# Performance work log

Hardware: AMD Instinct MI355X
Metric: run time of the kernel (lower is better)

Reference implementation:

```python
import jax, jax.numpy as jnp
import numpy as np

B, S, D = 2, 2048, 4096
NH, NKV = 32, 8
HD = D // NH          # 128
NREP = NH // NKV      # 4
SCALE = HD ** -0.5


def setup_inputs() -> dict:
    key = jax.random.key(0)
    kx, kq, kk, kv, ko = jax.random.split(key, 5)
    s = 0.02
    return {
        "x": jax.random.normal(kx, (B, S, D), dtype=jnp.float32),
        "wq": jax.random.normal(kq, (D, NH * HD), dtype=jnp.float32) * s,
        "wk": jax.random.normal(kk, (D, NKV * HD), dtype=jnp.float32) * s,
        "wv": jax.random.normal(kv, (D, NKV * HD), dtype=jnp.float32) * s,
        "wo": jax.random.normal(ko, (NH * HD, D), dtype=jnp.float32) * s,
    }


def reference(x, wq, wk, wv, wo):
    b, s, _ = x.shape
    q = (x @ wq).reshape(b, s, NH, HD)    # b s h d
    k = (x @ wk).reshape(b, s, NKV, HD)   # b s kv d
    v = (x @ wv).reshape(b, s, NKV, HD)
    # GQA: repeat kv heads to match query heads
    k = jnp.repeat(k, NREP, axis=2)       # b s h d
    v = jnp.repeat(v, NREP, axis=2)
    scores = jnp.einsum("bihd,bjhd->bhij", q, k) * SCALE  # b h i j
    causal = jnp.tril(jnp.ones((s, s), dtype=bool))
    scores = jnp.where(causal, scores, jnp.finfo(scores.dtype).min)
    attn = jax.nn.softmax(scores, axis=-1)
    out = jnp.einsum("bhij,bjhd->bihd", attn, v)          # b s h d
    out = out.reshape(b, s, NH * HD)
    return out @ wo
```

## Files before the change

### kernel.cpp

```cpp
#include <hip/hip_runtime.h>
#include <cstdint>
#include <cstddef>

typedef __bf16 bf16x8 __attribute__((ext_vector_type(8)));
typedef float  f32x4  __attribute__((ext_vector_type(4)));
typedef unsigned short u16;

#define SCALE_F 0.08838834764831845f
#define QSCALE_F (0.08838834764831845f * 1.4426950408889634f)

__device__ __forceinline__ u16 f2bf(float f) {
  unsigned int u = __builtin_bit_cast(unsigned int, f);
  u += 0x7fffu + ((u >> 16) & 1u);
  return (u16)(u >> 16);
}

__device__ __forceinline__ unsigned cvt_pk_bf16(float lo, float hi) {
  unsigned r;
  asm("v_cvt_pk_bf16_f32 %0, %1, %2" : "=v"(r) : "v"(lo), "v"(hi));
  return r;
}

__device__ __forceinline__ void load_lds16(const void* g, void* l) {
  __builtin_amdgcn_global_load_lds((const __attribute__((address_space(1))) void*)g,
                                   (__attribute__((address_space(3))) void*)l,
                                   16, 0, 0);
}

__global__ __launch_bounds__(256) void prep_all(const float* __restrict__ x,
                                                const float* __restrict__ wq,
                                                const float* __restrict__ wk,
                                                const float* __restrict__ wv,
                                                const float* __restrict__ wo,
                                                u16* __restrict__ xb,
                                                u16* __restrict__ wqkvT,
                                                u16* __restrict__ woT) {
  __shared__ float tile[32][33];
  const int tid = threadIdx.x;
  int blk = blockIdx.x;
  if (blk < 2048) {
    int idx = blk * 256 + tid;
    const int n4 = 4096 * 4096 / 4;
    for (; idx < n4; idx += 2048 * 256) {
      float4 v = ((const float4*)x)[idx];
      uint2 pk;
      pk.x = (unsigned)f2bf(v.x) | ((unsigned)f2bf(v.y) << 16);
      pk.y = (unsigned)f2bf(v.z) | ((unsigned)f2bf(v.w) << 16);
      ((uint2*)xb)[idx] = pk;
    }
    return;
  }
  blk -= 2048;
  const float* in; u16* out; long C; int nbx; float scale;
  if (blk < 16384)      { in = wq; out = wqkvT;                          C = 4096; nbx = 128; scale = QSCALE_F; }
  else if (blk < 20480) { blk -= 16384; in = wk; out = wqkvT + (size_t)4096 * 4096; C = 1024; nbx = 32; scale = 1.f; }
  else if (blk < 24576) { blk -= 20480; in = wv; out = wqkvT + (size_t)5120 * 4096; C = 1024; nbx = 32; scale = 1.f; }
  else                  { blk -= 24576; in = wo; out = woT;              C = 4096; nbx = 128; scale = 1.f; }
  const long R = 4096;
  const int tx = tid & 31, ty = tid >> 5;
  const long c0 = (long)(blk % nbx) * 32, r0 = (long)(blk / nbx) * 32;
#pragma unroll
  for (int i = 0; i < 4; i++)
    tile[ty + i * 8][tx] = in[(r0 + ty + i * 8) * C + c0 + tx];
  __syncthreads();
#pragma unroll
  for (int i = 0; i < 4; i++)
    out[(c0 + ty + i * 8) * R + r0 + tx] = f2bf(tile[tx][ty + i * 8] * scale);
}

__global__ __launch_bounds__(256) void transpose_u16(const u16* __restrict__ in,
                                                     u16* __restrict__ out,
                                                     int R, int C, int ldi, int ldo) {
  __shared__ u16 tile[32][33];
  const int tx = threadIdx.x, ty = threadIdx.y;
  const long c0 = (long)blockIdx.x * 32, r0 = (long)blockIdx.y * 32;
#pragma unroll
  for (int i = 0; i < 4; i++)
    tile[ty + i * 8][tx] = in[(r0 + ty + i * 8) * (long)ldi + c0 + tx];
  __syncthreads();
#pragma unroll
  for (int i = 0; i < 4; i++)
    out[(c0 + ty + i * 8) * (long)ldo + r0 + tx] = tile[tx][ty + i * 8];
}

#define STGA(db, ks, KC) { int kc_ = (KC) < K ? (KC) : 0; \
    load_lds16(gA0 + kc_, &SA[db][ks][s0 * 8]); \
    load_lds16(gA1 + kc_, &SA[db][ks][s1 * 8]); }
#define STGB(db, ks, KC) { int kc_ = (KC) < K ? (KC) : 0; \
    load_lds16(gB0 + kc_, &SB[db][ks][s0 * 8]); \
    load_lds16(gB1 + kc_, &SB[db][ks][s1 * 8]); }

#define PH(MBc, AU, BU, DBn, KSn, MBn, AN, RDB, BN, STG, DOVM) { \
    STG; \
    if (DOVM) asm volatile("s_waitcnt vmcnt(8)"); \
    __builtin_amdgcn_s_barrier(); \
    _Pragma("unroll") for (int mm = 0; mm < 4; mm++) \
      AN[mm] = *(const bf16x8*)(&SA[DBn][KSn][aoff + (MBn + mm) * 512]); \
    if (RDB) { \
      _Pragma("unroll") for (int n = 0; n < 4; n++) \
        BN[n] = *(const bf16x8*)(&SB[DBn][KSn][boff + n * 512]); \
    } \
    __builtin_amdgcn_s_setprio(1); \
    _Pragma("unroll") for (int mm = 0; mm < 4; mm++) \
      _Pragma("unroll") for (int n = 0; n < 4; n++) \
        acc[MBc + mm][n] = __builtin_amdgcn_mfma_f32_16x16x32_bf16(AU[mm], BU[n], acc[MBc + mm][n], 0, 0, 0); \
    __builtin_amdgcn_s_setprio(0); \
  }

template <int BF16_OUT>
__global__ __launch_bounds__(512, 2) void gemm256(const u16* __restrict__ A,
                                                  const u16* __restrict__ Bt,
                                                  void* __restrict__ Cv,
                                                  int M, int N, int K, int NBX) {
  __shared__ u16 SA[2][2][8192];
  __shared__ u16 SB[2][2][8192];
  const int tid = threadIdx.x;
  const int lane = tid & 63;
  const int g = lane >> 4, r16 = lane & 15;
  const int wid = tid >> 6;
  const int wm = wid >> 2, wn = wid & 3;

  const int cpx = gridDim.x >> 3;
  const int lin = (blockIdx.x & 7) * cpx + (blockIdx.x >> 3);
  const long bm = (long)(lin / NBX) * 256;
  const long bn = (long)(lin % NBX) * 256;

  const int s0 = tid, s1 = 512 + tid;
  const int rp0 = s0 >> 3, ci0 = (s0 & 7) ^ (rp0 & 7);
  const int rp1 = s1 >> 3, ci1 = (s1 & 7) ^ (rp1 & 7);
  const long gr0 = rp0 * 2 + (ci0 >> 2), gc0 = (ci0 & 3) * 8;
  const long gr1 = rp1 * 2 + (ci1 >> 2), gc1 = (ci1 & 3) * 8;
  const u16* gA0 = A + (bm + gr0) * K + gc0;
  const u16* gA1 = A + (bm + gr1) * K + gc1;
  const u16* gB0 = Bt + (bn + gr0) * K + gc0;
  const u16* gB1 = Bt + (bn + gr1) * K + gc1;

  const int rA = wm * 128 + r16;
  const int aoff = (rA >> 1) * 64 + ((((rA & 1) << 2) + g) ^ ((rA >> 1) & 7)) * 8;
  const int rB = wn * 64 + r16;
  const int boff = (rB >> 1) * 64 + ((((rB & 1) << 2) + g) ^ ((rB >> 1) & 7)) * 8;

  f32x4 acc[8][4];
#pragma unroll
  for (int m = 0; m < 8; m++)
#pragma unroll
    for (int n = 0; n < 4; n++)
#pragma unroll
      for (int j = 0; j < 4; j++) acc[m][n][j] = 0.f;

  bf16x8 afrX[4], afrY[4], bfrX[4], bfrY[4];

  STGA(0, 0, 0); STGB(0, 0, 0);
  STGA(0, 1, 32); STGB(0, 1, 32);
  STGA(1, 0, 64); STGB(1, 0, 64);
  __builtin_amdgcn_sched_barrier(0);
  asm volatile("s_waitcnt vmcnt(0)" ::: "memory");
  __builtin_amdgcn_s_barrier();

#pragma unroll
  for (int mm = 0; mm < 4; mm++)
    afrX[mm] = *(const bf16x8*)(&SA[0][0][aoff + mm * 512]);
#pragma unroll
  for (int n = 0; n < 4; n++)
    bfrX[n] = *(const bf16x8*)(&SB[0][0][boff + n * 512]);

  for (int it = 0; it < K / 128; it++) {
    const int t0 = it * 128;
    PH(0, afrX, bfrX, 0, 0, 4, afrY, 0, bfrY, STGA(1, 1, t0 + 96), 0);
    PH(4, afrY, bfrX, 0, 1, 0, afrX, 1, bfrY, STGB(1, 1, t0 + 96), 1);
    PH(0, afrX, bfrY, 0, 1, 4, afrY, 0, bfrX, STGA(0, 0, t0 + 128), 0);
    PH(4, afrY, bfrY, 1, 0, 0, afrX, 1, bfrX, STGB(0, 0, t0 + 128), 1);
    PH(0, afrX, bfrX, 1, 0, 4, afrY, 0, bfrY, STGA(0, 1, t0 + 160), 0);
    PH(4, afrY, bfrX, 1, 1, 0, afrX, 1, bfrY, STGB(0, 1, t0 + 160), 1);
    PH(0, afrX, bfrY, 1, 1, 4, afrY, 0, bfrX, STGA(1, 0, t0 + 192), 0);
    PH(4, afrY, bfrY, 0, 0, 0, afrX, 1, bfrX, STGB(1, 0, t0 + 192), 1);
  }

  const long crow = bm + wm * 128 + g * 4;
  const long ccol = bn + wn * 64 + r16;
  if (BF16_OUT) {
    u16* C = (u16*)Cv;
#pragma unroll
    for (int m = 0; m < 8; m++)
#pragma unroll
      for (int n = 0; n < 4; n++)
#pragma unroll
        for (int j = 0; j < 4; j++)
          C[(crow + m * 16 + j) * (long)N + ccol + n * 16] = f2bf(acc[m][n][j]);
  } else {
    float* C = (float*)Cv;
#pragma unroll
    for (int m = 0; m < 8; m++)
#pragma unroll
      for (int n = 0; n < 4; n++)
#pragma unroll
        for (int j = 0; j < 4; j++)
          C[(crow + m * 16 + j) * (long)N + ccol + n * 16] = acc[m][n][j];
  }
}

__global__ __launch_bounds__(512, 4) void attn_fwd(const u16* __restrict__ QK,
                                                   const u16* __restrict__ VT,
                                                   u16* __restrict__ Og) {
  __shared__ u16 Ks[2][64 * 128];
  __shared__ u16 Vs[2][128 * 64];
  __shared__ u16 Ps[8][16 * 64];
  const int tid = threadIdx.x;
  const int lane = tid & 63;
  const int w = tid >> 6;
  const int g = lane >> 4, r16 = lane & 15;
  const int qtA = blockIdx.x;
  const int qtB = 15 - qtA;
  const int h = blockIdx.y, b = blockIdx.z;
  const int kvh = h >> 2;

  const u16* kcol   = QK + (long)b * 2048 * 6144 + 4096 + kvh * 128;
  const u16* vb_ptr = VT + (long)kvh * 128 * 4096 + (long)b * 2048;
  u16* pw = Ps[w];

  const int nktA = 2 * (qtA + 1);
  const int ntot = 34;

  int qbase = qtA * 128;
  int qlo = qbase + w * 16;
  int qrow = qlo + r16;

  bf16x8 qf[4];
  auto load_q = [&]() {
    const u16* qp = QK + ((long)(b * 2048 + qrow)) * 6144 + h * 128 + g * 8;
#pragma unroll
    for (int kc = 0; kc < 4; kc++) qf[kc] = *(const bf16x8*)(qp + kc * 32);
  };
  load_q();

  f32x4 oacc[8];
  float mrun, lrun;
  auto reinit = [&]() {
#pragma unroll
    for (int dt = 0; dt < 8; dt++)
#pragma unroll
      for (int j = 0; j < 4; j++) oacc[dt][j] = 0.f;
    mrun = -__builtin_inff();
    lrun = 0.f;
  };
  reinit();

  auto finalize = [&]() {
    float li[4];
#pragma unroll
    for (int j = 0; j < 4; j++)
      li[j] = 1.f / __shfl(lrun, (lane & 48) + g * 4 + j);
    u16* op = Og + ((long)(b * 2048 + qbase + w * 16 + g * 4)) * 4096 + h * 128 + r16;
#pragma unroll
    for (int dt = 0; dt < 8; dt++)
#pragma unroll
      for (int j = 0; j < 4; j++)
        op[(long)j * 4096 + dt * 16] = f2bf(oacc[dt][j] * li[j]);
  };

  auto stage = [&](int bf, int kb) {
#pragma unroll
    for (int i = 0; i < 2; i++) {
      int slot = i * 512 + tid;
      int r = slot >> 4, cs = slot & 15;
      int ck = (cs & 8) | ((cs ^ r) & 7);
      load_lds16(kcol + (long)(kb + r) * 6144 + ck * 8, &Ks[bf][slot * 8]);
      int d = slot >> 3, c8 = slot & 7;
      int cv = (c8 ^ d) & 7;
      load_lds16(vb_ptr + (long)d * 4096 + kb + cv * 8, &Vs[bf][slot * 8]);
    }
  };

  stage(0, 0);
  __syncthreads();
  int cur = 0;

  for (int i = 0; i < ntot; i++) {
    if (i == nktA) {
      finalize();
      qbase = qtB * 128;
      qlo = qbase + w * 16;
      qrow = qlo + r16;
      load_q();
      reinit();
    }
    const int kt = (i < nktA) ? i : i - nktA;
    const int kb = kt * 64;
    if (i + 1 < ntot) {
      const int ktn = (i + 1 < nktA) ? i + 1 : i + 1 - nktA;
      stage(cur ^ 1, ktn * 64);
    }

    if (kb <= qlo + 15) {
      const bool masked = (kb + 63 > qlo);

      f32x4 st[4];
#pragma unroll
      for (int t = 0; t < 4; t++)
#pragma unroll
        for (int j = 0; j < 4; j++) st[t][j] = 0.f;
#pragma unroll
      for (int t = 0; t < 4; t++) {
        const int r = t * 16 + r16;
#pragma unroll
        for (int kc = 0; kc < 4; kc++) {
          int c = kc * 4 + g;
          int cz = (c & 8) | ((c ^ r) & 7);
          bf16x8 kf = *(const bf16x8*)(&Ks[cur][r * 128 + cz * 8]);
          st[t] = __builtin_amdgcn_mfma_f32_16x16x32_bf16(kf, qf[kc], st[t], 0, 0, 0);
        }
      }

      float p[4][4];
      float tmax = -__builtin_inff();
#pragma unroll
      for (int t = 0; t < 4; t++)
#pragma unroll
        for (int j = 0; j < 4; j++) {
          float s = st[t][j];
          if (masked) {
            int kv = kb + t * 16 + g * 4 + j;
            s = (kv > qrow) ? -__builtin_inff() : s;
          }
          p[t][j] = s;
          tmax = fmaxf(tmax, s);
        }
      tmax = fmaxf(tmax, __shfl_xor(tmax, 16));
      tmax = fmaxf(tmax, __shfl_xor(tmax, 32));

      if (!__all(tmax <= mrun + 8.f)) {
        const float mnew = fmaxf(mrun, tmax);
        const float esc = exp2f(mrun - mnew);
        float es[4];
#pragma unroll
        for (int j = 0; j < 4; j++) es[j] = __shfl(esc, (lane & 48) + g * 4 + j);
#pragma unroll
        for (int dt = 0; dt < 8; dt++)
#pragma unroll
          for (int j = 0; j < 4; j++) oacc[dt][j] *= es[j];
        lrun *= esc;
        mrun = mnew;
      }
      float psum = 0.f;
#pragma unroll
      for (int t = 0; t < 4; t++)
#pragma unroll
        for (int j = 0; j < 4; j++) {
          float e = exp2f(p[t][j] - mrun);
          p[t][j] = e;
          psum += e;
        }
      psum += __shfl_xor(psum, 16);
      psum += __shfl_xor(psum, 32);
      lrun += psum;

#pragma unroll
      for (int t = 0; t < 4; t++)
#pragma unroll
        for (int pp = 0; pp < 2; pp++) {
          int kvl = t * 16 + g * 4 + pp * 2;
          unsigned val = cvt_pk_bf16(p[t][pp * 2], p[t][pp * 2 + 1]);
          int off = r16 * 128 + ((kvl * 2) ^ ((r16 & 7) << 4));
          *(unsigned int*)((char*)pw + off) = val;
        }

#pragma unroll
      for (int kc2 = 0; kc2 < 2; kc2++) {
        int c = kc2 * 4 + g;
        int cp = c ^ (r16 & 7);
        bf16x8 pa = *(const bf16x8*)(pw + r16 * 64 + cp * 8);
#pragma unroll
        for (int dt = 0; dt < 8; dt++) {
          int d = dt * 16 + r16;
          int cz = c ^ (d & 7);
          bf16x8 vf = *(const bf16x8*)(&Vs[cur][d * 64 + cz * 8]);
          oacc[dt] = __builtin_amdgcn_mfma_f32_16x16x32_bf16(pa, vf, oacc[dt], 0, 0, 0);
        }
      }
    }

    __syncthreads();
    cur ^= 1;
  }

  finalize();
}

extern "C" void kernel_launch(void* const* d_in, const int* in_sizes, int n_in,
                              void* d_out, int out_size, void* d_ws, size_t ws_size,
                              hipStream_t stream) {
  (void)in_sizes; (void)n_in; (void)out_size; (void)ws_size;
  const float* x  = (const float*)d_in[0];
  const float* wq = (const float*)d_in[1];
  const float* wk = (const float*)d_in[2];
  const float* wv = (const float*)d_in[3];
  const float* wo = (const float*)d_in[4];
  float* out = (float*)d_out;

  u16* xb     = (u16*)d_ws;
  u16* wqkvT  = xb    + (size_t)4096 * 4096;
  u16* woT    = wqkvT + (size_t)6144 * 4096;
  u16* qkv    = woT   + (size_t)4096 * 4096;
  u16* vT     = qkv   + (size_t)4096 * 6144;
  u16* attn   = xb;

  prep_all<<<43008, 256, 0, stream>>>(x, wq, wk, wv, wo, xb, wqkvT, woT);

  gemm256<1><<<384, 512, 0, stream>>>(xb, wqkvT, qkv, 4096, 6144, 4096, 24);
  transpose_u16<<<dim3(32, 128), dim3(32, 8), 0, stream>>>(qkv + 5120, vT, 4096, 1024, 6144, 4096);

  attn_fwd<<<dim3(8, 32, 2), 512, 0, stream>>>(qkv, vT, attn);

  gemm256<0><<<256, 512, 0, stream>>>(attn, woT, out, 4096, 4096, 4096, 16);
}
```

Measured before the change: 523.3 us.

## Widen weight-transpose tiles, remap attention grid for KV locality, split GEMM kernels

The weight transpose in prep_all now handles 64x32 tiles and writes packed pairs of bf16 values as 32-bit stores, which halves the block count and widens the stores. The attention launch moves to a 1D grid with an XCD-aware remap, so the four query heads sharing a KV head, together with their query tiles, land on the same XCD and can share K/V through L2. The GEMM template is wrapped in two separately named kernels, which is mostly cosmetic. Side effects include more LDS per prep block and some fragility in the blockIdx remapping.

```diff
diff --git a/kernel.cpp b/kernel.cpp
--- a/kernel.cpp
+++ b/kernel.cpp
@@ -35,7 +35,7 @@
                                                 u16* __restrict__ xb,
                                                 u16* __restrict__ wqkvT,
                                                 u16* __restrict__ woT) {
-  __shared__ float tile[32][33];
+  __shared__ float tile[64][33];
   const int tid = threadIdx.x;
   int blk = blockIdx.x;
   if (blk < 2048) {
@@ -52,20 +52,29 @@
   }
   blk -= 2048;
   const float* in; u16* out; long C; int nbx; float scale;
-  if (blk < 16384)      { in = wq; out = wqkvT;                          C = 4096; nbx = 128; scale = QSCALE_F; }
-  else if (blk < 20480) { blk -= 16384; in = wk; out = wqkvT + (size_t)4096 * 4096; C = 1024; nbx = 32; scale = 1.f; }
-  else if (blk < 24576) { blk -= 20480; in = wv; out = wqkvT + (size_t)5120 * 4096; C = 1024; nbx = 32; scale = 1.f; }
-  else                  { blk -= 24576; in = wo; out = woT;              C = 4096; nbx = 128; scale = 1.f; }
+  if (blk < 8192)       { in = wq; out = wqkvT;                            C = 4096; nbx = 128; scale = QSCALE_F; }
+  else if (blk < 10240) { blk -= 8192;  in = wk; out = wqkvT + (size_t)4096 * 4096; C = 1024; nbx = 32; scale = 1.f; }
+  else if (blk < 12288) { blk -= 10240; in = wv; out = wqkvT + (size_t)5120 * 4096; C = 1024; nbx = 32; scale = 1.f; }
+  else                  { blk -= 12288; in = wo; out = woT;                C = 4096; nbx = 128; scale = 1.f; }
   const long R = 4096;
-  const int tx = tid & 31, ty = tid >> 5;
-  const long c0 = (long)(blk % nbx) * 32, r0 = (long)(blk / nbx) * 32;
-#pragma unroll
-  for (int i = 0; i < 4; i++)
-    tile[ty + i * 8][tx] = in[(r0 + ty + i * 8) * C + c0 + tx];
+  const long c0 = (long)(blk % nbx) * 32, r0 = (long)(blk / nbx) * 64;
+  {
+    const int tx = tid & 31, ty = tid >> 5;
+#pragma unroll
+    for (int i = 0; i < 8; i++)
+      tile[ty + i * 8][tx] = in[(r0 + ty + i * 8) * C + c0 + tx];
+  }
   __syncthreads();
-#pragma unroll
-  for (int i = 0; i < 4; i++)
-    out[(c0 + ty + i * 8) * R + r0 + tx] = f2bf(tile[tx][ty + i * 8] * scale);
+  {
+    const int tx = tid & 31, cy = tid >> 5;
+#pragma unroll
+    for (int i = 0; i < 4; i++) {
+      int col = cy + i * 8;
+      unsigned val = (unsigned)f2bf(tile[2 * tx][col] * scale) |
+                     ((unsigned)f2bf(tile[2 * tx + 1][col] * scale) << 16);
+      *(unsigned*)&out[(c0 + col) * R + r0 + 2 * tx] = val;
+    }
+  }
 }
 
 __global__ __launch_bounds__(256) void transpose_u16(const u16* __restrict__ in,
@@ -90,7 +99,7 @@
     load_lds16(gB0 + kc_, &SB[db][ks][s0 * 8]); \
     load_lds16(gB1 + kc_, &SB[db][ks][s1 * 8]); }
 
-#define PH(MBc, AU, BU, DBn, KSn, MBn, AN, RDB, BN, STG, DOVM) { \
+#define PH(MBc, AU, BU, DBn, KSn, MBn, AN, RDB, BN_, STG, DOVM) { \
     STG; \
     if (DOVM) asm volatile("s_waitcnt vmcnt(8)"); \
     __builtin_amdgcn_s_barrier(); \
@@ -98,7 +107,7 @@
       AN[mm] = *(const bf16x8*)(&SA[DBn][KSn][aoff + (MBn + mm) * 512]); \
     if (RDB) { \
       _Pragma("unroll") for (int n = 0; n < 4; n++) \
-        BN[n] = *(const bf16x8*)(&SB[DBn][KSn][boff + n * 512]); \
+        BN_[n] = *(const bf16x8*)(&SB[DBn][KSn][boff + n * 512]); \
     } \
     __builtin_amdgcn_s_setprio(1); \
     _Pragma("unroll") for (int mm = 0; mm < 4; mm++) \
@@ -108,10 +117,10 @@
   }
 
 template <int BF16_OUT>
-__global__ __launch_bounds__(512, 2) void gemm256(const u16* __restrict__ A,
-                                                  const u16* __restrict__ Bt,
-                                                  void* __restrict__ Cv,
-                                                  int M, int N, int K, int NBX) {
+__device__ __forceinline__ void gemm_body(const u16* __restrict__ A,
+                                          const u16* __restrict__ Bt,
+                                          void* __restrict__ Cv,
+                                          int M, int N, int K, int NBX) {
   __shared__ u16 SA[2][2][8192];
   __shared__ u16 SB[2][2][8192];
   const int tid = threadIdx.x;
@@ -199,6 +208,19 @@
   }
 }
 
+__global__ __launch_bounds__(512, 2) void gemm_qkv(const u16* __restrict__ A,
+                                                   const u16* __restrict__ Bt,
+                                                   void* __restrict__ Cv,
+                                                   int M, int N, int K, int NBX) {
+  gemm_body<1>(A, Bt, Cv, M, N, K, NBX);
+}
+__global__ __launch_bounds__(512, 2) void gemm_wo(const u16* __restrict__ A,
+                                                  const u16* __restrict__ Bt,
+                                                  void* __restrict__ Cv,
+                                                  int M, int N, int K, int NBX) {
+  gemm_body<0>(A, Bt, Cv, M, N, K, NBX);
+}
+
 __global__ __launch_bounds__(512, 4) void attn_fwd(const u16* __restrict__ QK,
                                                    const u16* __restrict__ VT,
                                                    u16* __restrict__ Og) {
@@ -209,10 +231,15 @@
   const int lane = tid & 63;
   const int w = tid >> 6;
   const int g = lane >> 4, r16 = lane & 15;
-  const int qtA = blockIdx.x;
+
+  const int lin = (blockIdx.x & 7) * 64 + (blockIdx.x >> 3);
+  const int b = lin >> 8;
+  const int rem = lin & 255;
+  const int kvh = rem >> 5;
+  const int hrep = (rem & 31) >> 3;
+  const int qtA = rem & 7;
   const int qtB = 15 - qtA;
-  const int h = blockIdx.y, b = blockIdx.z;
-  const int kvh = h >> 2;
+  const int h = kvh * 4 + hrep;
 
   const u16* kcol   = QK + (long)b * 2048 * 6144 + 4096 + kvh * 128;
   const u16* vb_ptr = VT + (long)kvh * 128 * 4096 + (long)b * 2048;
@@ -404,12 +431,12 @@
   u16* vT     = qkv   + (size_t)4096 * 6144;
   u16* attn   = xb;
 
-  prep_all<<<43008, 256, 0, stream>>>(x, wq, wk, wv, wo, xb, wqkvT, woT);
-
-  gemm256<1><<<384, 512, 0, stream>>>(xb, wqkvT, qkv, 4096, 6144, 4096, 24);
+  prep_all<<<22528, 256, 0, stream>>>(x, wq, wk, wv, wo, xb, wqkvT, woT);
+
+  gemm_qkv<<<384, 512, 0, stream>>>(xb, wqkvT, qkv, 4096, 6144, 4096, 24);
   transpose_u16<<<dim3(32, 128), dim3(32, 8), 0, stream>>>(qkv + 5120, vT, 4096, 1024, 6144, 4096);
 
-  attn_fwd<<<dim3(8, 32, 2), 512, 0, stream>>>(qkv, vT, attn);
-
-  gemm256<0><<<256, 512, 0, stream>>>(attn, woT, out, 4096, 4096, 4096, 16);
-}
+  attn_fwd<<<512, 512, 0, stream>>>(qkv, vT, attn);
+
+  gemm_wo<<<256, 512, 0, stream>>>(attn, woT, out, 4096, 4096, 4096, 16);
+}
```

New measurement: 526.4 us. About the same (+0.6%).
